# Kernel optimization log

Measured on AMD Instinct MI355X. Metric: run time of the kernel, lower is better.

The kernel has to match this reference:

```python
import jax, jax.numpy as jnp
import numpy as np

B, T, C, H, L, V = 2, 1024, 768, 12, 12, 50257
D = C // H  # head size = 64
EPS = 1e-5


def _layer_norm(x, w, b):
    m = x.mean(-1, keepdims=True)
    v = x.var(-1, keepdims=True)
    return (x - m) * jax.lax.rsqrt(v + EPS) * w + b


def setup_inputs() -> dict:
    key = jax.random.key(0)
    ks = jax.random.split(key, 8)
    std = 0.02
    res_std = 0.02 * (2 * L) ** -0.5  # NANOGPT_SCALE_INIT
    rn = lambda k, shape, s: jax.random.normal(k, shape, jnp.float32) * s
    return dict(
        idx=jax.random.randint(ks[0], (B, T), 0, V),
        wte=rn(ks[1], (V, C), std),
        wpe=rn(ks[2], (T, C), std),
        ln1_w=jnp.ones((L, C), jnp.float32), ln1_b=jnp.zeros((L, C), jnp.float32),
        qkv_w=rn(ks[3], (L, C, 3 * C), std), qkv_b=jnp.zeros((L, 3 * C), jnp.float32),
        proj_w=rn(ks[4], (L, C, C), res_std), proj_b=jnp.zeros((L, C), jnp.float32),
        ln2_w=jnp.ones((L, C), jnp.float32), ln2_b=jnp.zeros((L, C), jnp.float32),
        fc_w=rn(ks[5], (L, C, 4 * C), std), fc_b=jnp.zeros((L, 4 * C), jnp.float32),
        fco_w=rn(ks[6], (L, 4 * C, C), res_std), fco_b=jnp.zeros((L, C), jnp.float32),
        lnf_w=jnp.ones((C,), jnp.float32), lnf_b=jnp.zeros((C,), jnp.float32),
    )


def reference(idx, wte, wpe, ln1_w, ln1_b, qkv_w, qkv_b, proj_w, proj_b,
              ln2_w, ln2_b, fc_w, fc_b, fco_w, fco_b, lnf_w, lnf_b):
    x = wte[idx] + wpe[:T]  # [B, T, C] tok + pos emb
    mask = jnp.tril(jnp.ones((T, T), bool))  # causal
    scale = 1.0 / np.sqrt(D).astype(np.float32)

    def block(x, p):
        l1w, l1b, qw, qb, pw, pb, l2w, l2b, fw, fb, fow, fob = p
        h = _layer_norm(x, l1w, l1b)
        qkv = h @ qw + qb  # [B, T, 3C]
        q, k, v = jnp.split(qkv, 3, axis=-1)
        q = q.reshape(B, T, H, D)
        k = k.reshape(B, T, H, D)
        v = v.reshape(B, T, H, D)
        att = jnp.einsum('bqhd,bkhd->bhqk', q, k) * scale
        att = jnp.where(mask, att, -jnp.inf)
        att = jax.nn.softmax(att, axis=-1)
        y = jnp.einsum('bhqk,bkhd->bqhd', att, v).reshape(B, T, C)
        x = x + y @ pw + pb
        h2 = _layer_norm(x, l2w, l2b)
        x = x + jax.nn.gelu(h2 @ fw + fb, approximate=True) @ fow + fob
        return x, None

    x, _ = jax.lax.scan(block, x, (ln1_w, ln1_b, qkv_w, qkv_b, proj_w, proj_b,
                                   ln2_w, ln2_b, fc_w, fc_b, fco_w, fco_b))
    x = _layer_norm(x, lnf_w, lnf_b)
    logits = x @ wte.T  # tied lm_head
    return logits
```

## Files before the change

kernel.cpp:

```cpp
#include <hip/hip_runtime.h>
#include <cmath>
#include <cstdint>

#define T_SEQ 1024
#define NH 12
#define NL 12
#define NV 50257
#define CD 768
#define M_ROWS 2048

typedef __bf16 bf16_t;
typedef __bf16 bf16x8 __attribute__((ext_vector_type(8)));
typedef float f32x4 __attribute__((ext_vector_type(4)));

__device__ __forceinline__ void gload16(const bf16_t* g, bf16_t* l) {
  __builtin_amdgcn_global_load_lds(
      (const __attribute__((address_space(1))) void*)g,
      (__attribute__((address_space(3))) void*)l, 16, 0, 0);
}

__global__ __launch_bounds__(256) void embed_k(const int* __restrict__ idx,
    const float* __restrict__ wte, const float* __restrict__ wpe,
    float* __restrict__ x) {
  int m = blockIdx.x;
  int t = m & (T_SEQ - 1);
  int tok = idx[m];
  const float* a = wte + (size_t)tok * CD;
  const float* p = wpe + (size_t)t * CD;
  float* xr = x + (size_t)m * CD;
  int c = threadIdx.x;
  xr[c]       = a[c]       + p[c];
  xr[c + 256] = a[c + 256] + p[c + 256];
  xr[c + 512] = a[c + 512] + p[c + 512];
}

__global__ __launch_bounds__(256) void cvt_k(const float* __restrict__ in,
    bf16_t* __restrict__ out, int n4) {
  int i = blockIdx.x * 256 + threadIdx.x;
  if (i < n4) {
    float4 v = ((const float4*)in)[i];
    bf16_t* o = out + (size_t)i * 4;
    o[0] = (bf16_t)v.x; o[1] = (bf16_t)v.y;
    o[2] = (bf16_t)v.z; o[3] = (bf16_t)v.w;
  }
}

__global__ __launch_bounds__(256) void transcvt_k(const float* __restrict__ W0,
    bf16_t* __restrict__ WT0, int K, int N) {
  const float* W = W0 + (size_t)blockIdx.z * K * N;
  bf16_t* WT = WT0 + (size_t)blockIdx.z * N * K;
  __shared__ float tl[32][33];
  int k0 = blockIdx.y * 32, n0 = blockIdx.x * 32;
  int j = threadIdx.x & 31, i0 = threadIdx.x >> 5;
  #pragma unroll
  for (int i = i0; i < 32; i += 8) tl[i][j] = W[(size_t)(k0 + i) * N + n0 + j];
  __syncthreads();
  #pragma unroll
  for (int i = i0; i < 32; i += 8)
    WT[(size_t)(n0 + i) * K + k0 + j] = (bf16_t)tl[j][i];
}

__global__ __launch_bounds__(256) void ln_k(const float* __restrict__ x,
    const float* __restrict__ w, const float* __restrict__ bi,
    bf16_t* __restrict__ out) {
  int row = blockIdx.x;
  const float* xr = x + (size_t)row * CD;
  int t = threadIdx.x;
  float v0 = xr[t], v1 = xr[t + 256], v2 = xr[t + 512];
  float s = v0 + v1 + v2;
  float ss = v0 * v0 + v1 * v1 + v2 * v2;
  #pragma unroll
  for (int o = 1; o < 64; o <<= 1) { s += __shfl_xor(s, o); ss += __shfl_xor(ss, o); }
  __shared__ float sh[8];
  int wid = t >> 6, lane = t & 63;
  if (lane == 0) { sh[wid] = s; sh[4 + wid] = ss; }
  __syncthreads();
  s  = sh[0] + sh[1] + sh[2] + sh[3];
  ss = sh[4] + sh[5] + sh[6] + sh[7];
  float mean = s * (1.f / CD);
  float var  = ss * (1.f / CD) - mean * mean;
  float rs = rsqrtf(var + 1e-5f);
  bf16_t* orow = out + (size_t)row * CD;
  orow[t]       = (bf16_t)((v0 - mean) * rs * w[t]       + bi[t]);
  orow[t + 256] = (bf16_t)((v1 - mean) * rs * w[t + 256] + bi[t + 256]);
  orow[t + 512] = (bf16_t)((v2 - mean) * rs * w[t + 512] + bi[t + 512]);
}

template <int BM, int BN, int EPI, bool SWAP, bool XSWZ>
__global__ __launch_bounds__(256) void gemm_bt(
    const bf16_t* __restrict__ A,
    const bf16_t* __restrict__ BT,
    const float* __restrict__ bias,
    const float* __restrict__ resid,
    void* __restrict__ out_p,
    int Mdim, int Ndim, int Kdim) {
  constexpr int MR = BM / 32, NR = BN / 32;
  constexpr int LPW = (BM + BN) / 64;
  __shared__ __align__(1024) bf16_t As[3][BM * 32];
  __shared__ __align__(1024) bf16_t Bs[3][BN * 32];
  const int t = threadIdx.x;
  const int wid = t >> 6, lane = t & 63;
  const int wm = wid >> 1, wn = wid & 1;
  int bx = blockIdx.x, by = blockIdx.y;
  if (XSWZ) {
    int gx = gridDim.x;
    int lin = by * gx + bx;
    int cpx = (gx * gridDim.y) >> 3;
    int swz = (lin & 7) * cpx + (lin >> 3);
    bx = swz % gx; by = swz / gx;
  }
  const int m0 = (SWAP ? bx : by) * BM;
  const int n0 = (SWAP ? by : bx) * BN;
  const int l15 = lane & 15, lhi = lane >> 4;

  const int srow = lane >> 2;
  const int schk = lane & 3;

  auto stage = [&](int bi, int kt) {
    #pragma unroll
    for (int i = 0; i < BM / 64; ++i) {
      int rbase = wid * (BM / 4) + i * 16;
      int r = rbase + srow;
      int c = schk ^ ((r >> 1) & 3);
      gload16(A + (size_t)(m0 + r) * Kdim + kt + c * 8, &As[bi][rbase * 32]);
    }
    #pragma unroll
    for (int i = 0; i < BN / 64; ++i) {
      int rbase = wid * (BN / 4) + i * 16;
      int r = rbase + srow;
      int nr = n0 + r; if (nr >= Ndim) nr = Ndim - 1;
      int c = schk ^ ((r >> 1) & 3);
      gload16(BT + (size_t)nr * Kdim + kt + c * 8, &Bs[bi][rbase * 32]);
    }
  };

  f32x4 acc[MR][NR] = {};
  const int NT = Kdim >> 5;

  stage(0, 0);
  if (NT > 1) stage(1, 32);
  for (int tt = 0; tt < NT; ++tt) {
    if (tt < NT - 1) asm volatile("s_waitcnt vmcnt(%0)" :: "i"(LPW) : "memory");
    else             asm volatile("s_waitcnt vmcnt(0)" ::: "memory");
    __builtin_amdgcn_sched_barrier(0);
    __builtin_amdgcn_s_barrier();
    __builtin_amdgcn_sched_barrier(0);

    const bf16_t* Ab = As[tt % 3];
    const bf16_t* Bb = Bs[tt % 3];
    bf16x8 af[MR], bfr[NR];
    #pragma unroll
    for (int mm = 0; mm < MR; ++mm) {
      int ra = wm * (BM / 2) + mm * 16 + l15;
      af[mm] = *(const bf16x8*)&Ab[ra * 32 + ((lhi ^ (ra >> 1)) & 3) * 8];
    }
    #pragma unroll
    for (int nn = 0; nn < NR; ++nn) {
      int rb = wn * (BN / 2) + nn * 16 + l15;
      bfr[nn] = *(const bf16x8*)&Bb[rb * 32 + ((lhi ^ (rb >> 1)) & 3) * 8];
    }
    if (tt + 2 < NT) stage((tt + 2) % 3, (tt + 2) * 32);

    __builtin_amdgcn_s_setprio(1);
    #pragma unroll
    for (int mm = 0; mm < MR; ++mm)
      #pragma unroll
      for (int nn = 0; nn < NR; ++nn)
        acc[mm][nn] = __builtin_amdgcn_mfma_f32_16x16x32_bf16(af[mm], bfr[nn], acc[mm][nn], 0, 0, 0);
    __builtin_amdgcn_s_setprio(0);

    __builtin_amdgcn_sched_barrier(0);
    __builtin_amdgcn_s_barrier();
    __builtin_amdgcn_sched_barrier(0);
  }

  bf16_t* ob = (bf16_t*)out_p;
  float*  of = (float*)out_p;
  const int row0 = m0 + wm * (BM / 2);
  const int col0 = n0 + wn * (BN / 2);
  #pragma unroll
  for (int mm = 0; mm < MR; ++mm) {
    #pragma unroll
    for (int nn = 0; nn < NR; ++nn) {
      int col = col0 + nn * 16 + l15;
      if (col >= Ndim) continue;
      float bv = (EPI != 3) ? bias[col] : 0.f;
      #pragma unroll
      for (int r = 0; r < 4; ++r) {
        int row = row0 + mm * 16 + lhi * 4 + r;
        float v = acc[mm][nn][r] + bv;
        size_t o = (size_t)row * Ndim + col;
        if (EPI == 0) {
          ob[o] = (bf16_t)v;
        } else if (EPI == 1) {
          float u = v + 0.044715f * v * v * v;
          v = 0.5f * v * (1.f + tanhf(0.79788456080286536f * u));
          ob[o] = (bf16_t)v;
        } else if (EPI == 2) {
          of[o] = resid[o] + v;
        } else {
          of[o] = v;
        }
      }
    }
  }
}

__global__ __launch_bounds__(256) void vtrans_k(const bf16_t* __restrict__ qkv,
                                                bf16_t* __restrict__ VT) {
  __shared__ __align__(16) bf16_t tl[64 * 72];
  const int bh = blockIdx.y;
  const int t0 = blockIdx.x * 64;
  const int b = bh / NH, h = bh % NH;
  const int tid = threadIdx.x;
  const int row = tid >> 2;
  const int seg = (tid & 3) * 16;

  const bf16_t* src = qkv + (size_t)(b * T_SEQ + t0 + row) * (3 * CD) + 2 * CD + h * 64 + seg;
  bf16x8 v0 = *(const bf16x8*)src;
  bf16x8 v1 = *(const bf16x8*)(src + 8);
  #pragma unroll
  for (int j = 0; j < 8; ++j) tl[(seg + j) * 72 + row] = v0[j];
  #pragma unroll
  for (int j = 0; j < 8; ++j) tl[(seg + 8 + j) * 72 + row] = v1[j];
  __syncthreads();

  bf16_t* dst = VT + ((size_t)bh * 64 + row) * T_SEQ + t0 + seg;
  *(bf16x8*)dst       = *(const bf16x8*)&tl[row * 72 + seg];
  *(bf16x8*)(dst + 8) = *(const bf16x8*)&tl[row * 72 + seg + 8];
}

__global__ __launch_bounds__(64) void attn_k(const bf16_t* __restrict__ qkv,
                                             const bf16_t* __restrict__ VT,
                                             bf16_t* __restrict__ y) {
  __shared__ __align__(16) bf16_t Ps[16 * 40];
  const int lane = threadIdx.x;
  const int gw = blockIdx.x;
  const int qi = gw & 63;
  const int bh = gw >> 6;
  const int h = bh % NH, b = bh / NH;
  const bf16_t* Qbase = qkv + (size_t)b * T_SEQ * (3 * CD) + h * 64;
  const bf16_t* Kbase = Qbase + CD;
  const bf16_t* Vt = VT + (size_t)bh * 64 * T_SEQ;

  const int l15 = lane & 15, lhi = lane >> 4;
  const int q0 = qi * 16;

  bf16x8 aq[2];
  #pragma unroll
  for (int c = 0; c < 2; ++c)
    aq[c] = *(const bf16x8*)(Qbase + (size_t)(q0 + l15) * (3 * CD) + c * 32 + lhi * 8);

  f32x4 acc[4] = {};
  float m_[4], l_[4];
  #pragma unroll
  for (int r = 0; r < 4; ++r) { m_[r] = -INFINITY; l_[r] = 0.f; }

  const int qrow = q0 + lhi * 4;
  const int nt = (q0 + 47) / 32;
  for (int kt = 0; kt < nt; ++kt) {
    const int k0 = kt * 32;
    f32x4 s[2] = {};
    #pragma unroll
    for (int c = 0; c < 2; ++c) {
      #pragma unroll
      for (int kc = 0; kc < 2; ++kc) {
        bf16x8 bk = *(const bf16x8*)(Kbase + (size_t)(k0 + kc * 16 + l15) * (3 * CD) + c * 32 + lhi * 8);
        s[kc] = __builtin_amdgcn_mfma_f32_16x16x32_bf16(aq[c], bk, s[kc], 0, 0, 0);
      }
    }
    float mx[4];
    #pragma unroll
    for (int r = 0; r < 4; ++r) mx[r] = -INFINITY;
    #pragma unroll
    for (int kc = 0; kc < 2; ++kc) {
      const int kcol = k0 + kc * 16 + l15;
      #pragma unroll
      for (int r = 0; r < 4; ++r) {
        float sv = (kcol <= qrow + r) ? s[kc][r] * 0.125f : -INFINITY;
        s[kc][r] = sv;
        mx[r] = fmaxf(mx[r], sv);
      }
    }
    #pragma unroll
    for (int r = 0; r < 4; ++r) {
      mx[r] = fmaxf(mx[r], __shfl_xor(mx[r], 1));
      mx[r] = fmaxf(mx[r], __shfl_xor(mx[r], 2));
      mx[r] = fmaxf(mx[r], __shfl_xor(mx[r], 4));
      mx[r] = fmaxf(mx[r], __shfl_xor(mx[r], 8));
    }
    float al[4], rs[4];
    #pragma unroll
    for (int r = 0; r < 4; ++r) {
      float mn = fmaxf(m_[r], mx[r]);
      al[r] = __expf(m_[r] - mn);
      m_[r] = mn;
      float p0 = __expf(s[0][r] - mn);
      float p1 = __expf(s[1][r] - mn);
      s[0][r] = p0; s[1][r] = p1;
      rs[r] = p0 + p1;
    }
    #pragma unroll
    for (int r = 0; r < 4; ++r) {
      rs[r] += __shfl_xor(rs[r], 1);
      rs[r] += __shfl_xor(rs[r], 2);
      rs[r] += __shfl_xor(rs[r], 4);
      rs[r] += __shfl_xor(rs[r], 8);
      l_[r] = l_[r] * al[r] + rs[r];
    }
    #pragma unroll
    for (int dt = 0; dt < 4; ++dt)
      #pragma unroll
      for (int r = 0; r < 4; ++r) acc[dt][r] *= al[r];
    #pragma unroll
    for (int kc = 0; kc < 2; ++kc)
      #pragma unroll
      for (int r = 0; r < 4; ++r)
        Ps[(lhi * 4 + r) * 40 + kc * 16 + l15] = (bf16_t)s[kc][r];
    bf16x8 pa = *(const bf16x8*)&Ps[l15 * 40 + lhi * 8];
    #pragma unroll
    for (int dt = 0; dt < 4; ++dt) {
      bf16x8 bv = *(const bf16x8*)(Vt + (size_t)(dt * 16 + l15) * T_SEQ + k0 + lhi * 8);
      acc[dt] = __builtin_amdgcn_mfma_f32_16x16x32_bf16(pa, bv, acc[dt], 0, 0, 0);
    }
  }
  #pragma unroll
  for (int dt = 0; dt < 4; ++dt)
    #pragma unroll
    for (int r = 0; r < 4; ++r)
      y[(size_t)(b * T_SEQ + q0 + lhi * 4 + r) * CD + h * 64 + dt * 16 + l15] =
          (bf16_t)(acc[dt][r] / l_[r]);
}

extern "C" void kernel_launch(void* const* d_in, const int* in_sizes, int n_in,
                              void* d_out, int out_size, void* d_ws, size_t ws_size,
                              hipStream_t stream) {
  const int*   idx   = (const int*)d_in[0];
  const float* wte   = (const float*)d_in[1];
  const float* wpe   = (const float*)d_in[2];
  const float* ln1w  = (const float*)d_in[3];
  const float* ln1b  = (const float*)d_in[4];
  const float* qkvw  = (const float*)d_in[5];
  const float* qkvb  = (const float*)d_in[6];
  const float* projw = (const float*)d_in[7];
  const float* projb = (const float*)d_in[8];
  const float* ln2w  = (const float*)d_in[9];
  const float* ln2b  = (const float*)d_in[10];
  const float* fcw   = (const float*)d_in[11];
  const float* fcb   = (const float*)d_in[12];
  const float* fcow  = (const float*)d_in[13];
  const float* fcob  = (const float*)d_in[14];
  const float* lnfw  = (const float*)d_in[15];
  const float* lnfb  = (const float*)d_in[16];
  float* out = (float*)d_out;

  char* w = (char*)d_ws;
  auto alloc = [&](size_t bytes) {
    char* p = w; w += (bytes + 255) & ~(size_t)255; return p;
  };
  float*  x    = (float*)alloc((size_t)M_ROWS * CD * 4);
  float*  x2   = (float*)alloc((size_t)M_ROWS * CD * 4);
  bf16_t* hb   = (bf16_t*)alloc((size_t)M_ROWS * CD * 2);
  bf16_t* qkvB = (bf16_t*)alloc((size_t)M_ROWS * 3 * CD * 2);
  bf16_t* yb   = (bf16_t*)alloc((size_t)M_ROWS * CD * 2);
  bf16_t* fca  = (bf16_t*)alloc((size_t)M_ROWS * 4 * CD * 2);
  bf16_t* VT   = (bf16_t*)alloc((size_t)2 * NH * 64 * T_SEQ * 2);
  bf16_t* wteB = (bf16_t*)alloc((size_t)NV * CD * 2);
  bf16_t* wqT_s = (bf16_t*)alloc((size_t)3 * CD * CD * 2);
  bf16_t* wpT_s = (bf16_t*)alloc((size_t)CD * CD * 2);
  bf16_t* wfT_s = (bf16_t*)alloc((size_t)4 * CD * CD * 2);
  bf16_t* woT_s = (bf16_t*)alloc((size_t)CD * 4 * CD * 2);
  const size_t qkvSz = (size_t)3 * CD * CD, prSz = (size_t)CD * CD;
  const size_t fcSz  = (size_t)4 * CD * CD, foSz = (size_t)CD * 4 * CD;
  bf16_t* wqT_b = (bf16_t*)alloc(NL * qkvSz * 2);
  bf16_t* wpT_b = (bf16_t*)alloc(NL * prSz * 2);
  bf16_t* wfT_b = (bf16_t*)alloc(NL * fcSz * 2);
  bf16_t* woT_b = (bf16_t*)alloc(NL * foSz * 2);
  const bool big = (size_t)(w - (char*)d_ws) <= ws_size;

  embed_k<<<M_ROWS, 256, 0, stream>>>(idx, wte, wpe, x);
  {
    int n4 = NV * CD / 4;
    cvt_k<<<(n4 + 255) / 256, 256, 0, stream>>>(wte, wteB, n4);
  }
  if (big) {
    transcvt_k<<<dim3(3 * CD / 32, CD / 32, NL), 256, 0, stream>>>(qkvw,  wqT_b, CD, 3 * CD);
    transcvt_k<<<dim3(CD / 32, CD / 32, NL),     256, 0, stream>>>(projw, wpT_b, CD, CD);
    transcvt_k<<<dim3(4 * CD / 32, CD / 32, NL), 256, 0, stream>>>(fcw,   wfT_b, CD, 4 * CD);
    transcvt_k<<<dim3(CD / 32, 4 * CD / 32, NL), 256, 0, stream>>>(fcow,  woT_b, 4 * CD, CD);
  }

  for (int l = 0; l < NL; ++l) {
    bf16_t *wqT, *wpT, *wfT, *woT;
    if (big) {
      wqT = wqT_b + (size_t)l * qkvSz; wpT = wpT_b + (size_t)l * prSz;
      wfT = wfT_b + (size_t)l * fcSz;  woT = woT_b + (size_t)l * foSz;
    } else {
      wqT = wqT_s; wpT = wpT_s; wfT = wfT_s; woT = woT_s;
      transcvt_k<<<dim3(3 * CD / 32, CD / 32, 1), 256, 0, stream>>>(qkvw  + (size_t)l * CD * 3 * CD, wqT, CD, 3 * CD);
      transcvt_k<<<dim3(CD / 32, CD / 32, 1),     256, 0, stream>>>(projw + (size_t)l * CD * CD,     wpT, CD, CD);
      transcvt_k<<<dim3(4 * CD / 32, CD / 32, 1), 256, 0, stream>>>(fcw   + (size_t)l * CD * 4 * CD, wfT, CD, 4 * CD);
      transcvt_k<<<dim3(CD / 32, 4 * CD / 32, 1), 256, 0, stream>>>(fcow  + (size_t)l * 4 * CD * CD, woT, 4 * CD, CD);
    }

    ln_k<<<M_ROWS, 256, 0, stream>>>(x, ln1w + l * CD, ln1b + l * CD, hb);
    gemm_bt<128, 128, 0, false, false><<<dim3(3 * CD / 128, M_ROWS / 128), 256, 0, stream>>>(
        hb, wqT, qkvb + l * 3 * CD, nullptr, qkvB, M_ROWS, 3 * CD, CD);
    vtrans_k<<<dim3(T_SEQ / 64, 2 * NH), 256, 0, stream>>>(qkvB, VT);
    attn_k<<<2 * NH * 64, 64, 0, stream>>>(qkvB, VT, yb);
    gemm_bt<64, 64, 2, false, false><<<dim3(CD / 64, M_ROWS / 64), 256, 0, stream>>>(
        yb, wpT, projb + l * CD, x, x2, M_ROWS, CD, CD);
    ln_k<<<M_ROWS, 256, 0, stream>>>(x2, ln2w + l * CD, ln2b + l * CD, hb);
    gemm_bt<128, 128, 1, false, false><<<dim3(4 * CD / 128, M_ROWS / 128), 256, 0, stream>>>(
        hb, wfT, fcb + l * 4 * CD, nullptr, fca, M_ROWS, 4 * CD, CD);
    gemm_bt<64, 64, 2, false, false><<<dim3(CD / 64, M_ROWS / 64), 256, 0, stream>>>(
        fca, woT, fcob + l * CD, x2, x, M_ROWS, CD, 4 * CD);
  }

  ln_k<<<M_ROWS, 256, 0, stream>>>(x, lnfw, lnfb, hb);
  gemm_bt<128, 128, 3, true, true><<<dim3(16, (NV + 127) / 128), 256, 0, stream>>>(
      hb, wteB, nullptr, nullptr, out, M_ROWS, NV, CD);
}
```

Measured before the change: 2.322 ms.

## Fuse V transpose into QKV GEMM, split-K FC-out, widen attention key tiles

The QKV GEMM epilogue now writes the V columns straight into the transposed VT buffer, which removes the separate vtrans kernel. The FC-output GEMM becomes a 4-way split-K GEMM writing fp32 partial sums, and a new add-reduce kernel adds residual, bias and partials to raise parallelism for that narrow GEMM. The attention kernel processes 64 keys per iteration instead of 32, which halves the loop trip count. In exchange the split-K path adds 4x fp32 partial traffic plus an extra launch, and the VT stores from the GEMM epilogue are scattered 8-byte writes.

```diff
diff --git a/kernel.cpp b/kernel.cpp
--- a/kernel.cpp
+++ b/kernel.cpp
@@ -10,6 +10,7 @@
 #define M_ROWS 2048
 
 typedef __bf16 bf16_t;
+typedef __bf16 bf16x4 __attribute__((ext_vector_type(4)));
 typedef __bf16 bf16x8 __attribute__((ext_vector_type(8)));
 typedef float f32x4 __attribute__((ext_vector_type(4)));
 
@@ -86,14 +87,34 @@
   orow[t + 512] = (bf16_t)((v2 - mean) * rs * w[t + 512] + bi[t + 512]);
 }
 
-template <int BM, int BN, int EPI, bool SWAP, bool XSWZ>
+__global__ __launch_bounds__(256) void addred_k(const float* __restrict__ x2,
+    const float* __restrict__ bias, const float* __restrict__ part,
+    float* __restrict__ xo) {
+  const int NF4 = M_ROWS * CD / 4;
+  int i = blockIdx.x * 256 + threadIdx.x;
+  float4 r  = ((const float4*)x2)[i];
+  float4 b  = ((const float4*)bias)[i % (CD / 4)];
+  float4 p0 = ((const float4*)part)[i];
+  float4 p1 = ((const float4*)part)[i + NF4];
+  float4 p2 = ((const float4*)part)[i + 2 * NF4];
+  float4 p3 = ((const float4*)part)[i + 3 * NF4];
+  float4 o;
+  o.x = r.x + b.x + ((p0.x + p1.x) + (p2.x + p3.x));
+  o.y = r.y + b.y + ((p0.y + p1.y) + (p2.y + p3.y));
+  o.z = r.z + b.z + ((p0.z + p1.z) + (p2.z + p3.z));
+  o.w = r.w + b.w + ((p0.w + p1.w) + (p2.w + p3.w));
+  ((float4*)xo)[i] = o;
+}
+
+template <int BM, int BN, int EPI, bool SWAP, bool XSWZ, bool PARTK>
 __global__ __launch_bounds__(256) void gemm_bt(
     const bf16_t* __restrict__ A,
     const bf16_t* __restrict__ BT,
     const float* __restrict__ bias,
     const float* __restrict__ resid,
     void* __restrict__ out_p,
-    int Mdim, int Ndim, int Kdim) {
+    bf16_t* __restrict__ vt,
+    int Mdim, int Ndim, int Kdim, int ldA, int ldB) {
   constexpr int MR = BM / 32, NR = BN / 32;
   constexpr int LPW = (BM + BN) / 64;
   __shared__ __align__(1024) bf16_t As[3][BM * 32];
@@ -109,6 +130,10 @@
     int swz = (lin & 7) * cpx + (lin >> 3);
     bx = swz % gx; by = swz / gx;
   }
+  if (PARTK) {
+    A  += (size_t)blockIdx.z * Kdim;
+    BT += (size_t)blockIdx.z * Kdim;
+  }
   const int m0 = (SWAP ? bx : by) * BM;
   const int n0 = (SWAP ? by : bx) * BN;
   const int l15 = lane & 15, lhi = lane >> 4;
@@ -122,7 +147,7 @@
       int rbase = wid * (BM / 4) + i * 16;
       int r = rbase + srow;
       int c = schk ^ ((r >> 1) & 3);
-      gload16(A + (size_t)(m0 + r) * Kdim + kt + c * 8, &As[bi][rbase * 32]);
+      gload16(A + (size_t)(m0 + r) * ldA + kt + c * 8, &As[bi][rbase * 32]);
     }
     #pragma unroll
     for (int i = 0; i < BN / 64; ++i) {
@@ -130,7 +155,7 @@
       int r = rbase + srow;
       int nr = n0 + r; if (nr >= Ndim) nr = Ndim - 1;
       int c = schk ^ ((r >> 1) & 3);
-      gload16(BT + (size_t)nr * Kdim + kt + c * 8, &Bs[bi][rbase * 32]);
+      gload16(BT + (size_t)nr * ldB + kt + c * 8, &Bs[bi][rbase * 32]);
     }
   };
 
@@ -176,6 +201,7 @@
 
   bf16_t* ob = (bf16_t*)out_p;
   float*  of = (float*)out_p;
+  if (PARTK) of += (size_t)blockIdx.z * Mdim * Ndim;
   const int row0 = m0 + wm * (BM / 2);
   const int col0 = n0 + wn * (BN / 2);
   #pragma unroll
@@ -185,55 +211,48 @@
       int col = col0 + nn * 16 + l15;
       if (col >= Ndim) continue;
       float bv = (EPI != 3) ? bias[col] : 0.f;
-      #pragma unroll
-      for (int r = 0; r < 4; ++r) {
-        int row = row0 + mm * 16 + lhi * 4 + r;
-        float v = acc[mm][nn][r] + bv;
-        size_t o = (size_t)row * Ndim + col;
-        if (EPI == 0) {
-          ob[o] = (bf16_t)v;
-        } else if (EPI == 1) {
-          float u = v + 0.044715f * v * v * v;
-          v = 0.5f * v * (1.f + tanhf(0.79788456080286536f * u));
-          ob[o] = (bf16_t)v;
-        } else if (EPI == 2) {
-          of[o] = resid[o] + v;
-        } else {
-          of[o] = v;
+      if (EPI == 0) {
+        bf16_t vv[4];
+        #pragma unroll
+        for (int r = 0; r < 4; ++r) {
+          int row = row0 + mm * 16 + lhi * 4 + r;
+          float v = acc[mm][nn][r] + bv;
+          vv[r] = (bf16_t)v;
+          ob[(size_t)row * Ndim + col] = vv[r];
+        }
+        if (vt != nullptr && col >= 2 * CD) {
+          int h = (col - 2 * CD) >> 6;
+          int d = (col - 2 * CD) & 63;
+          int brow = row0 + mm * 16 + lhi * 4;
+          int bh = (brow >> 10) * NH + h;
+          int tt0 = brow & (T_SEQ - 1);
+          *(bf16x4*)&vt[((size_t)bh * 64 + d) * T_SEQ + tt0] = *(const bf16x4*)vv;
+        }
+      } else {
+        #pragma unroll
+        for (int r = 0; r < 4; ++r) {
+          int row = row0 + mm * 16 + lhi * 4 + r;
+          float v = acc[mm][nn][r] + bv;
+          size_t o = (size_t)row * Ndim + col;
+          if (EPI == 1) {
+            float u = v + 0.044715f * v * v * v;
+            v = 0.5f * v * (1.f + tanhf(0.79788456080286536f * u));
+            ob[o] = (bf16_t)v;
+          } else if (EPI == 2) {
+            of[o] = resid[o] + v;
+          } else {
+            of[o] = v;
+          }
         }
       }
     }
   }
-}
-
-__global__ __launch_bounds__(256) void vtrans_k(const bf16_t* __restrict__ qkv,
-                                                bf16_t* __restrict__ VT) {
-  __shared__ __align__(16) bf16_t tl[64 * 72];
-  const int bh = blockIdx.y;
-  const int t0 = blockIdx.x * 64;
-  const int b = bh / NH, h = bh % NH;
-  const int tid = threadIdx.x;
-  const int row = tid >> 2;
-  const int seg = (tid & 3) * 16;
-
-  const bf16_t* src = qkv + (size_t)(b * T_SEQ + t0 + row) * (3 * CD) + 2 * CD + h * 64 + seg;
-  bf16x8 v0 = *(const bf16x8*)src;
-  bf16x8 v1 = *(const bf16x8*)(src + 8);
-  #pragma unroll
-  for (int j = 0; j < 8; ++j) tl[(seg + j) * 72 + row] = v0[j];
-  #pragma unroll
-  for (int j = 0; j < 8; ++j) tl[(seg + 8 + j) * 72 + row] = v1[j];
-  __syncthreads();
-
-  bf16_t* dst = VT + ((size_t)bh * 64 + row) * T_SEQ + t0 + seg;
-  *(bf16x8*)dst       = *(const bf16x8*)&tl[row * 72 + seg];
-  *(bf16x8*)(dst + 8) = *(const bf16x8*)&tl[row * 72 + seg + 8];
 }
 
 __global__ __launch_bounds__(64) void attn_k(const bf16_t* __restrict__ qkv,
                                              const bf16_t* __restrict__ VT,
                                              bf16_t* __restrict__ y) {
-  __shared__ __align__(16) bf16_t Ps[16 * 40];
+  __shared__ __align__(16) bf16_t Ps[16 * 72];
   const int lane = threadIdx.x;
   const int gw = blockIdx.x;
   const int qi = gw & 63;
@@ -257,14 +276,14 @@
   for (int r = 0; r < 4; ++r) { m_[r] = -INFINITY; l_[r] = 0.f; }
 
   const int qrow = q0 + lhi * 4;
-  const int nt = (q0 + 47) / 32;
+  const int nt = (q0 + 79) / 64;
   for (int kt = 0; kt < nt; ++kt) {
-    const int k0 = kt * 32;
-    f32x4 s[2] = {};
+    const int k0 = kt * 64;
+    f32x4 s[4] = {};
     #pragma unroll
     for (int c = 0; c < 2; ++c) {
       #pragma unroll
-      for (int kc = 0; kc < 2; ++kc) {
+      for (int kc = 0; kc < 4; ++kc) {
         bf16x8 bk = *(const bf16x8*)(Kbase + (size_t)(k0 + kc * 16 + l15) * (3 * CD) + c * 32 + lhi * 8);
         s[kc] = __builtin_amdgcn_mfma_f32_16x16x32_bf16(aq[c], bk, s[kc], 0, 0, 0);
       }
@@ -273,7 +292,7 @@
     #pragma unroll
     for (int r = 0; r < 4; ++r) mx[r] = -INFINITY;
     #pragma unroll
-    for (int kc = 0; kc < 2; ++kc) {
+    for (int kc = 0; kc < 4; ++kc) {
       const int kcol = k0 + kc * 16 + l15;
       #pragma unroll
       for (int r = 0; r < 4; ++r) {
@@ -297,8 +316,10 @@
       m_[r] = mn;
       float p0 = __expf(s[0][r] - mn);
       float p1 = __expf(s[1][r] - mn);
-      s[0][r] = p0; s[1][r] = p1;
-      rs[r] = p0 + p1;
+      float p2 = __expf(s[2][r] - mn);
+      float p3 = __expf(s[3][r] - mn);
+      s[0][r] = p0; s[1][r] = p1; s[2][r] = p2; s[3][r] = p3;
+      rs[r] = (p0 + p1) + (p2 + p3);
     }
     #pragma unroll
     for (int r = 0; r < 4; ++r) {
@@ -313,15 +334,18 @@
       #pragma unroll
       for (int r = 0; r < 4; ++r) acc[dt][r] *= al[r];
     #pragma unroll
-    for (int kc = 0; kc < 2; ++kc)
+    for (int kc = 0; kc < 4; ++kc)
       #pragma unroll
       for (int r = 0; r < 4; ++r)
-        Ps[(lhi * 4 + r) * 40 + kc * 16 + l15] = (bf16_t)s[kc][r];
-    bf16x8 pa = *(const bf16x8*)&Ps[l15 * 40 + lhi * 8];
-    #pragma unroll
-    for (int dt = 0; dt < 4; ++dt) {
-      bf16x8 bv = *(const bf16x8*)(Vt + (size_t)(dt * 16 + l15) * T_SEQ + k0 + lhi * 8);
-      acc[dt] = __builtin_amdgcn_mfma_f32_16x16x32_bf16(pa, bv, acc[dt], 0, 0, 0);
+        Ps[(lhi * 4 + r) * 72 + kc * 16 + l15] = (bf16_t)s[kc][r];
+    #pragma unroll
+    for (int ks = 0; ks < 2; ++ks) {
+      bf16x8 pa = *(const bf16x8*)&Ps[l15 * 72 + ks * 32 + lhi * 8];
+      #pragma unroll
+      for (int dt = 0; dt < 4; ++dt) {
+        bf16x8 bv = *(const bf16x8*)(Vt + (size_t)(dt * 16 + l15) * T_SEQ + k0 + ks * 32 + lhi * 8);
+        acc[dt] = __builtin_amdgcn_mfma_f32_16x16x32_bf16(pa, bv, acc[dt], 0, 0, 0);
+      }
     }
   }
   #pragma unroll
@@ -358,14 +382,15 @@
   auto alloc = [&](size_t bytes) {
     char* p = w; w += (bytes + 255) & ~(size_t)255; return p;
   };
-  float*  x    = (float*)alloc((size_t)M_ROWS * CD * 4);
-  float*  x2   = (float*)alloc((size_t)M_ROWS * CD * 4);
-  bf16_t* hb   = (bf16_t*)alloc((size_t)M_ROWS * CD * 2);
-  bf16_t* qkvB = (bf16_t*)alloc((size_t)M_ROWS * 3 * CD * 2);
-  bf16_t* yb   = (bf16_t*)alloc((size_t)M_ROWS * CD * 2);
-  bf16_t* fca  = (bf16_t*)alloc((size_t)M_ROWS * 4 * CD * 2);
-  bf16_t* VT   = (bf16_t*)alloc((size_t)2 * NH * 64 * T_SEQ * 2);
-  bf16_t* wteB = (bf16_t*)alloc((size_t)NV * CD * 2);
+  float*  x     = (float*)alloc((size_t)M_ROWS * CD * 4);
+  float*  x2    = (float*)alloc((size_t)M_ROWS * CD * 4);
+  bf16_t* hb    = (bf16_t*)alloc((size_t)M_ROWS * CD * 2);
+  bf16_t* qkvB  = (bf16_t*)alloc((size_t)M_ROWS * 3 * CD * 2);
+  bf16_t* yb    = (bf16_t*)alloc((size_t)M_ROWS * CD * 2);
+  bf16_t* fca   = (bf16_t*)alloc((size_t)M_ROWS * 4 * CD * 2);
+  bf16_t* VT    = (bf16_t*)alloc((size_t)2 * NH * 64 * T_SEQ * 2);
+  float*  fpart = (float*)alloc((size_t)4 * M_ROWS * CD * 4);
+  bf16_t* wteB  = (bf16_t*)alloc((size_t)NV * CD * 2);
   bf16_t* wqT_s = (bf16_t*)alloc((size_t)3 * CD * CD * 2);
   bf16_t* wpT_s = (bf16_t*)alloc((size_t)CD * CD * 2);
   bf16_t* wfT_s = (bf16_t*)alloc((size_t)4 * CD * CD * 2);
@@ -404,20 +429,20 @@
     }
 
     ln_k<<<M_ROWS, 256, 0, stream>>>(x, ln1w + l * CD, ln1b + l * CD, hb);
-    gemm_bt<128, 128, 0, false, false><<<dim3(3 * CD / 128, M_ROWS / 128), 256, 0, stream>>>(
-        hb, wqT, qkvb + l * 3 * CD, nullptr, qkvB, M_ROWS, 3 * CD, CD);
-    vtrans_k<<<dim3(T_SEQ / 64, 2 * NH), 256, 0, stream>>>(qkvB, VT);
+    gemm_bt<128, 128, 0, false, false, false><<<dim3(3 * CD / 128, M_ROWS / 128), 256, 0, stream>>>(
+        hb, wqT, qkvb + l * 3 * CD, nullptr, qkvB, VT, M_ROWS, 3 * CD, CD, CD, CD);
     attn_k<<<2 * NH * 64, 64, 0, stream>>>(qkvB, VT, yb);
-    gemm_bt<64, 64, 2, false, false><<<dim3(CD / 64, M_ROWS / 64), 256, 0, stream>>>(
-        yb, wpT, projb + l * CD, x, x2, M_ROWS, CD, CD);
+    gemm_bt<64, 64, 2, false, false, false><<<dim3(CD / 64, M_ROWS / 64), 256, 0, stream>>>(
+        yb, wpT, projb + l * CD, x, x2, nullptr, M_ROWS, CD, CD, CD, CD);
     ln_k<<<M_ROWS, 256, 0, stream>>>(x2, ln2w + l * CD, ln2b + l * CD, hb);
-    gemm_bt<128, 128, 1, false, false><<<dim3(4 * CD / 128, M_ROWS / 128), 256, 0, stream>>>(
-        hb, wfT, fcb + l * 4 * CD, nullptr, fca, M_ROWS, 4 * CD, CD);
-    gemm_bt<64, 64, 2, false, false><<<dim3(CD / 64, M_ROWS / 64), 256, 0, stream>>>(
-        fca, woT, fcob + l * CD, x2, x, M_ROWS, CD, 4 * CD);
+    gemm_bt<128, 128, 1, false, false, false><<<dim3(4 * CD / 128, M_ROWS / 128), 256, 0, stream>>>(
+        hb, wfT, fcb + l * 4 * CD, nullptr, fca, nullptr, M_ROWS, 4 * CD, CD, CD, CD);
+    gemm_bt<64, 64, 3, false, false, true><<<dim3(CD / 64, M_ROWS / 64, 4), 256, 0, stream>>>(
+        fca, woT, nullptr, nullptr, fpart, nullptr, M_ROWS, CD, CD, 4 * CD, 4 * CD);
+    addred_k<<<M_ROWS * CD / 1024, 256, 0, stream>>>(x2, fcob + l * CD, fpart, x);
   }
 
   ln_k<<<M_ROWS, 256, 0, stream>>>(x, lnfw, lnfb, hb);
-  gemm_bt<128, 128, 3, true, true><<<dim3(16, (NV + 127) / 128), 256, 0, stream>>>(
-      hb, wteB, nullptr, nullptr, out, M_ROWS, NV, CD);
-}
+  gemm_bt<128, 128, 3, true, true, false><<<dim3(16, (NV + 127) / 128), 256, 0, stream>>>(
+      hb, wteB, nullptr, nullptr, out, nullptr, M_ROWS, NV, CD, CD, CD);
+}
```

After: 2.449 ms. 1.05x slower.
